# Optimization experiments

Hardware: AMD Instinct MI355X
Metric: run time of the kernel (lower is better)

## Reference

```python
import jax, jax.numpy as jnp
import numpy as np

B, NV, NH = 4096, 128, 64


def setup_inputs() -> dict:
    key = jax.random.key(0)
    ks = jax.random.split(key, 8)
    return {
        "muvTE": jax.random.normal(ks[0], (B, NV), dtype=jnp.float32),
        "varvhTE": jax.random.normal(ks[1], (B, NH, NV), dtype=jnp.float32),
        "varh_diagTE": jax.random.normal(ks[2], (B, NH), dtype=jnp.float32),
        # strictly positive: it is inverted (diag(1/varh_diag))
        "varh_diag": jax.random.uniform(ks[3], (B, NH), dtype=jnp.float32, minval=0.5, maxval=1.5),
        "muh": jax.random.normal(ks[4], (B, NH), dtype=jnp.float32),
        "varvh": jax.random.normal(ks[5], (B, NH, NV), dtype=jnp.float32),
        "muhTE": jax.random.normal(ks[6], (B, NH), dtype=jnp.float32),
        "varvbarTE": jax.random.normal(ks[7], (B,), dtype=jnp.float32),
        "nv": NV,
    }


def reference(muvTE, varvhTE, varh_diagTE, varh_diag, muh, varvh, muhTE, varvbarTE, nv):
    # varh_inv and varhTE are diagonal matrices in the original TF code; we
    # apply them as broadcast vector scalings (same math, no [B,nh,nh] diags).
    vinv = 1.0 / varh_diag                      # [B,nh] (= diag of varh_inv)
    inner1 = vinv * muh                         # varh_inv @ muh
    inner2 = vinv * varh_diagTE * inner1        # varh_inv @ varhTE @ varh_inv @ muh
    inner3 = vinv * muhTE                       # varh_inv @ muhTE

    # bTE = muvTE - varvhTE^T (vinv muh) + varvh^T (vinv dTE vinv muh) - varvh^T (vinv muhTE)
    bTE = (muvTE
           - jnp.einsum('bhv,bh->bv', varvhTE, inner1)
           + jnp.einsum('bhv,bh->bv', varvh, inner2)
           - jnp.einsum('bhv,bh->bv', varvh, inner3))

    # wtTE = -varh_inv varhTE varh_inv varvh + varh_inv varvhTE   -> [B,nh,nv]
    wtTE = (-(vinv * varh_diagTE * vinv)[:, :, None] * varvh
            + vinv[:, :, None] * varvhTE)

    # trace(sig2TEmat) without materializing the [B,nv,nv] matrix:
    # tr(A^T D B) = sum_{h,v} A[h,v] * d[h] * B[h,v]
    tr = (jnp.einsum('bhv,bh,bhv->b', varvhTE, vinv, varvh)
          - jnp.einsum('bhv,bh,bhv->b', varvh, vinv * varh_diagTE * vinv, varvh)
          + jnp.einsum('bhv,bh,bhv->b', varvh, vinv, varvhTE))
    sig2TE = (varvbarTE - tr) / nv

    return bTE, wtTE, sig2TE, muhTE, varh_diagTE
```

## Files before the change

kernel.cpp:

```cpp
#include <hip/hip_runtime.h>

#define B_  4096
#define NH_ 64
#define NV_ 128

__global__ __launch_bounds__(256)
void cpmte_kernel(const float* __restrict__ muvTE,
                  const float* __restrict__ varvhTE,
                  const float* __restrict__ varh_diagTE,
                  const float* __restrict__ varh_diag,
                  const float* __restrict__ muh,
                  const float* __restrict__ varvh,
                  const float* __restrict__ muhTE,
                  const float* __restrict__ varvbarTE,
                  const int*   __restrict__ nv_p,
                  float* __restrict__ out_bTE,
                  float* __restrict__ out_wtTE,
                  float* __restrict__ out_sig2,
                  float* __restrict__ out_muhTE,
                  float* __restrict__ out_vdTE)
{
    const int b   = blockIdx.x;
    const int tid = threadIdx.x;

    __shared__ float s_inner1[NH_];
    __shared__ float s_d23[NH_];
    __shared__ float s_wA[NH_];
    __shared__ float s_vinv[NH_];
    __shared__ float s_bpart[8][NV_];
    __shared__ float s_tr[4];

    if (tid < NH_) {
        const int h = tid;
        const float vd   = varh_diag  [(size_t)b * NH_ + h];
        const float vinv = 1.0f / vd;
        const float vdTE = varh_diagTE[(size_t)b * NH_ + h];
        const float m    = muh        [(size_t)b * NH_ + h];
        const float mTE  = muhTE      [(size_t)b * NH_ + h];
        const float inner1 = vinv * m;
        const float inner2 = vinv * vdTE * inner1;
        const float inner3 = vinv * mTE;
        s_inner1[h] = inner1;
        s_d23[h]    = inner2 - inner3;
        s_wA[h]     = -vinv * vinv * vdTE;
        s_vinv[h]   = vinv;
        out_muhTE[(size_t)b * NH_ + h] = mTE;
        out_vdTE [(size_t)b * NH_ + h] = vdTE;
    }
    __syncthreads();

    const int lane_v = tid & 31;
    const int grp    = tid >> 5;

    const float4* TEp = (const float4*)(varvhTE + (size_t)b * NH_ * NV_);
    const float4* VHp = (const float4*)(varvh   + (size_t)b * NH_ * NV_);
    float4*       WTp = (float4*)(out_wtTE + (size_t)b * NH_ * NV_);

    float4 accb = make_float4(0.f, 0.f, 0.f, 0.f);
    float  tr   = 0.f;

    #pragma unroll
    for (int k = 0; k < 8; ++k) {
        const int h   = grp * 8 + k;
        const int idx = h * (NV_ / 4) + lane_v;
        const float4 te = TEp[idx];
        const float4 vh = VHp[idx];
        const float i1  = s_inner1[h];
        const float d23 = s_d23[h];
        const float wA  = s_wA[h];
        const float vi  = s_vinv[h];

        accb.x += d23 * vh.x - i1 * te.x;
        accb.y += d23 * vh.y - i1 * te.y;
        accb.z += d23 * vh.z - i1 * te.z;
        accb.w += d23 * vh.w - i1 * te.w;

        float4 wt;
        wt.x = wA * vh.x + vi * te.x;
        wt.y = wA * vh.y + vi * te.y;
        wt.z = wA * vh.z + vi * te.z;
        wt.w = wA * vh.w + vi * te.w;
        WTp[idx] = wt;

        tr += vh.x * (2.f * vi * te.x + wA * vh.x);
        tr += vh.y * (2.f * vi * te.y + wA * vh.y);
        tr += vh.z * (2.f * vi * te.z + wA * vh.z);
        tr += vh.w * (2.f * vi * te.w + wA * vh.w);
    }

    ((float4*)s_bpart[grp])[lane_v] = accb;

    #pragma unroll
    for (int off = 32; off >= 1; off >>= 1)
        tr += __shfl_down(tr, off, 64);
    if ((tid & 63) == 0) s_tr[tid >> 6] = tr;

    __syncthreads();

    if (tid < NV_) {
        float s = muvTE[(size_t)b * NV_ + tid];
        #pragma unroll
        for (int g = 0; g < 8; ++g) s += s_bpart[g][tid];
        out_bTE[(size_t)b * NV_ + tid] = s;
    }
    if (tid == 0) {
        const float t = s_tr[0] + s_tr[1] + s_tr[2] + s_tr[3];
        out_sig2[b] = (varvbarTE[b] - t) / (float)nv_p[0];
    }
}

extern "C" void kernel_launch(void* const* d_in, const int* in_sizes, int n_in,
                              void* d_out, int out_size, void* d_ws, size_t ws_size,
                              hipStream_t stream) {
    const float* muvTE       = (const float*)d_in[0];
    const float* varvhTE     = (const float*)d_in[1];
    const float* varh_diagTE = (const float*)d_in[2];
    const float* varh_diag   = (const float*)d_in[3];
    const float* muh         = (const float*)d_in[4];
    const float* varvh       = (const float*)d_in[5];
    const float* muhTE       = (const float*)d_in[6];
    const float* varvbarTE   = (const float*)d_in[7];
    const int*   nv_p        = (const int*)d_in[8];

    float* out = (float*)d_out;
    float* out_bTE   = out;
    float* out_wtTE  = out_bTE  + (size_t)B_ * NV_;
    float* out_sig2  = out_wtTE + (size_t)B_ * NH_ * NV_;
    float* out_muhTE = out_sig2 + (size_t)B_;
    float* out_vdTE  = out_muhTE + (size_t)B_ * NH_;

    dim3 grid(B_), block(256);
    cpmte_kernel<<<grid, block, 0, stream>>>(muvTE, varvhTE, varh_diagTE, varh_diag,
                                             muh, varvh, muhTE, varvbarTE, nv_p,
                                             out_bTE, out_wtTE, out_sig2,
                                             out_muhTE, out_vdTE);
}
```

Baseline: 79.99 us.

## Map one batch per half-wavefront and drop shared-memory reductions

```diff
diff --git a/kernel.cpp b/kernel.cpp
--- a/kernel.cpp
+++ b/kernel.cpp
@@ -3,6 +3,8 @@
 #define B_  4096
 #define NH_ 64
 #define NV_ 128
+
+typedef float nfloat4 __attribute__((ext_vector_type(4)));
 
 __global__ __launch_bounds__(256)
 void cpmte_kernel(const float* __restrict__ muvTE,
@@ -20,93 +22,68 @@
                   float* __restrict__ out_muhTE,
                   float* __restrict__ out_vdTE)
 {
-    const int b   = blockIdx.x;
-    const int tid = threadIdx.x;
+    const int tid  = threadIdx.x;
+    const int lane = tid & 63;
+    const int wv   = tid >> 6;
+    const int b    = blockIdx.x * 8 + wv * 2 + (lane >> 5);
+    const int v4   = lane & 31;
 
-    __shared__ float s_inner1[NH_];
-    __shared__ float s_d23[NH_];
-    __shared__ float s_wA[NH_];
-    __shared__ float s_vinv[NH_];
-    __shared__ float s_bpart[8][NV_];
-    __shared__ float s_tr[4];
+    {
+        const size_t base = (size_t)blockIdx.x * 8 * NH_;
+        out_muhTE[base + tid]       = muhTE[base + tid];
+        out_muhTE[base + tid + 256] = muhTE[base + tid + 256];
+        out_vdTE [base + tid]       = varh_diagTE[base + tid];
+        out_vdTE [base + tid + 256] = varh_diagTE[base + tid + 256];
+    }
 
-    if (tid < NH_) {
-        const int h = tid;
-        const float vd   = varh_diag  [(size_t)b * NH_ + h];
-        const float vinv = 1.0f / vd;
-        const float vdTE = varh_diagTE[(size_t)b * NH_ + h];
-        const float m    = muh        [(size_t)b * NH_ + h];
-        const float mTE  = muhTE      [(size_t)b * NH_ + h];
-        const float inner1 = vinv * m;
-        const float inner2 = vinv * vdTE * inner1;
-        const float inner3 = vinv * mTE;
-        s_inner1[h] = inner1;
-        s_d23[h]    = inner2 - inner3;
-        s_wA[h]     = -vinv * vinv * vdTE;
-        s_vinv[h]   = vinv;
-        out_muhTE[(size_t)b * NH_ + h] = mTE;
-        out_vdTE [(size_t)b * NH_ + h] = vdTE;
+    const nfloat4* TEp = (const nfloat4*)(varvhTE + (size_t)b * NH_ * NV_);
+    const nfloat4* VHp = (const nfloat4*)(varvh   + (size_t)b * NH_ * NV_);
+    nfloat4*       WTp = (nfloat4*)(out_wtTE + (size_t)b * NH_ * NV_);
+
+    const float* vdp   = varh_diag   + (size_t)b * NH_;
+    const float* vdTEp = varh_diagTE + (size_t)b * NH_;
+    const float* mp    = muh         + (size_t)b * NH_;
+    const float* mTEp  = muhTE       + (size_t)b * NH_;
+
+    nfloat4 accb = ((const nfloat4*)(muvTE + (size_t)b * NV_))[v4];
+    float tr = 0.f;
+
+    #pragma unroll 8
+    for (int h = 0; h < NH_; ++h) {
+        const nfloat4 t4 = TEp[h * (NV_ / 4) + v4];
+        const nfloat4 vh = VHp[h * (NV_ / 4) + v4];
+
+        const float vinv = 1.0f / vdp[h];
+        const float vdTE = vdTEp[h];
+        const float i1   = vinv * mp[h];
+        const float d23  = vinv * (vdTE * i1 - mTEp[h]);
+        const float wA   = -vinv * vinv * vdTE;
+
+        accb.x += d23 * vh.x - i1 * t4.x;
+        accb.y += d23 * vh.y - i1 * t4.y;
+        accb.z += d23 * vh.z - i1 * t4.z;
+        accb.w += d23 * vh.w - i1 * t4.w;
+
+        nfloat4 wt;
+        wt.x = wA * vh.x + vinv * t4.x;
+        wt.y = wA * vh.y + vinv * t4.y;
+        wt.z = wA * vh.z + vinv * t4.z;
+        wt.w = wA * vh.w + vinv * t4.w;
+        __builtin_nontemporal_store(wt, &WTp[h * (NV_ / 4) + v4]);
+
+        tr += vh.x * (2.f * vinv * t4.x + wA * vh.x);
+        tr += vh.y * (2.f * vinv * t4.y + wA * vh.y);
+        tr += vh.z * (2.f * vinv * t4.z + wA * vh.z);
+        tr += vh.w * (2.f * vinv * t4.w + wA * vh.w);
     }
-    __syncthreads();
 
-    const int lane_v = tid & 31;
-    const int grp    = tid >> 5;
-
-    const float4* TEp = (const float4*)(varvhTE + (size_t)b * NH_ * NV_);
-    const float4* VHp = (const float4*)(varvh   + (size_t)b * NH_ * NV_);
-    float4*       WTp = (float4*)(out_wtTE + (size_t)b * NH_ * NV_);
-
-    float4 accb = make_float4(0.f, 0.f, 0.f, 0.f);
-    float  tr   = 0.f;
+    ((nfloat4*)(out_bTE + (size_t)b * NV_))[v4] = accb;
 
     #pragma unroll
-    for (int k = 0; k < 8; ++k) {
-        const int h   = grp * 8 + k;
-        const int idx = h * (NV_ / 4) + lane_v;
-        const float4 te = TEp[idx];
-        const float4 vh = VHp[idx];
-        const float i1  = s_inner1[h];
-        const float d23 = s_d23[h];
-        const float wA  = s_wA[h];
-        const float vi  = s_vinv[h];
-
-        accb.x += d23 * vh.x - i1 * te.x;
-        accb.y += d23 * vh.y - i1 * te.y;
-        accb.z += d23 * vh.z - i1 * te.z;
-        accb.w += d23 * vh.w - i1 * te.w;
-
-        float4 wt;
-        wt.x = wA * vh.x + vi * te.x;
-        wt.y = wA * vh.y + vi * te.y;
-        wt.z = wA * vh.z + vi * te.z;
-        wt.w = wA * vh.w + vi * te.w;
-        WTp[idx] = wt;
-
-        tr += vh.x * (2.f * vi * te.x + wA * vh.x);
-        tr += vh.y * (2.f * vi * te.y + wA * vh.y);
-        tr += vh.z * (2.f * vi * te.z + wA * vh.z);
-        tr += vh.w * (2.f * vi * te.w + wA * vh.w);
-    }
-
-    ((float4*)s_bpart[grp])[lane_v] = accb;
-
-    #pragma unroll
-    for (int off = 32; off >= 1; off >>= 1)
-        tr += __shfl_down(tr, off, 64);
-    if ((tid & 63) == 0) s_tr[tid >> 6] = tr;
-
-    __syncthreads();
-
-    if (tid < NV_) {
-        float s = muvTE[(size_t)b * NV_ + tid];
-        #pragma unroll
-        for (int g = 0; g < 8; ++g) s += s_bpart[g][tid];
-        out_bTE[(size_t)b * NV_ + tid] = s;
-    }
-    if (tid == 0) {
-        const float t = s_tr[0] + s_tr[1] + s_tr[2] + s_tr[3];
-        out_sig2[b] = (varvbarTE[b] - t) / (float)nv_p[0];
-    }
+    for (int off = 16; off >= 1; off >>= 1)
+        tr += __shfl_down(tr, off, 32);
+    if (v4 == 0)
+        out_sig2[b] = (varvbarTE[b] - tr) / (float)nv_p[0];
 }
 
 extern "C" void kernel_launch(void* const* d_in, const int* in_sizes, int n_in,
@@ -129,7 +106,7 @@
     float* out_muhTE = out_sig2 + (size_t)B_;
     float* out_vdTE  = out_muhTE + (size_t)B_ * NH_;
 
-    dim3 grid(B_), block(256);
+    dim3 grid(B_ / 8), block(256);
     cpmte_kernel<<<grid, block, 0, stream>>>(muvTE, varvhTE, varh_diagTE, varh_diag,
                                              muh, varvh, muhTE, varvbarTE, nv_p,
                                              out_bTE, out_wtTE, out_sig2,
```

After: 85.52 us. +6.9%, slower.
